# Optimization experiments

Hardware: AMD Instinct MI355X
Metric: run time of the kernel (lower is better)

The kernel has to match this reference:

```python
import jax, jax.numpy as jnp
import numpy as np

HEADS, HEAD_DIM, NQP, NVP = 12, 16, 4, 8
NODE_DIM, EDGE_DIM = 384, 128
B, N = 1, 768


def setup_inputs() -> dict:
    key = jax.random.key(0)
    ks = jax.random.split(key, 12)
    node_features = jax.random.normal(ks[0], (B, N, NODE_DIM), dtype=jnp.float32)
    edge_features = jax.random.normal(ks[1], (B, N, N, EDGE_DIM), dtype=jnp.float32)
    # random valid rotations via QR of gaussian matrices (well-conditioned for inverse)
    A = jax.random.normal(ks[2], (B, N, 3, 3), dtype=jnp.float32)
    Q, _ = jnp.linalg.qr(A)
    R = Q
    t = jax.random.normal(ks[3], (B, N, 3), dtype=jnp.float32)
    def lin(k, din, dout):
        return jax.random.normal(k, (din, dout), dtype=jnp.float32) / np.sqrt(din)
    Wqkv = lin(ks[4], NODE_DIM, 3 * HEADS * HEAD_DIM)
    Wvqk = lin(ks[5], NODE_DIM, 2 * 3 * NQP * HEADS)
    Wvv = lin(ks[6], NODE_DIM, 3 * NVP * HEADS)
    Webias = lin(ks[7], EDGE_DIM, HEADS)
    fin_in = HEADS * EDGE_DIM + HEADS * HEAD_DIM + HEADS * NVP * 4
    Wfin = lin(ks[8], fin_in, NODE_DIM)
    bfin = jnp.zeros((NODE_DIM,), dtype=jnp.float32)
    return {"node_features": node_features, "edge_features": edge_features,
            "R": R, "t": t, "Wqkv": Wqkv, "Wvqk": Wvqk, "Wvv": Wvv,
            "Webias": Webias, "Wfin": Wfin, "bfin": bfin}


def _ipa(node_features, edge_features, R, t, Wqkv, Wvqk, Wvv, Webias, Wfin, bfin):
    b, n, _ = node_features.shape
    h, d, p, pv = HEADS, HEAD_DIM, NQP, NVP
    # scalar q, k, v: [b, h, n, d]
    qkv = (node_features @ Wqkv).reshape(b, n, 3, h, d)
    sq, sk, sv = [jnp.transpose(qkv[:, :, i], (0, 2, 1, 3)) for i in range(3)]
    node_scalar = jnp.einsum('bhid,bhjd->bhij', sq, sk) * (d ** -0.5)
    edge_bias = jnp.einsum('bijd,dh->bhij', edge_features, Webias)
    # vector q/k in local frames: [b, h, n, p, 3]
    vqk = (node_features @ Wvqk).reshape(b, n, 2, h, p, 3)
    vq = jnp.transpose(vqk[:, :, 0], (0, 2, 1, 3, 4))
    vk = jnp.transpose(vqk[:, :, 1], (0, 2, 1, 3, 4))
    t_e = t[:, None, :, None, :]  # [b,1,n,1,3]
    gq = jnp.einsum('bnij,bhnpj->bhnpi', R, vq) + t_e
    gk = jnp.einsum('bnij,bhnpj->bhnpi', R, vk) + t_e
    # ||gk_i - gq_j||^2 summed over (p,3), expanded to avoid [b,h,n,n,p,3]
    wc = np.sqrt(2.0 / 9.0 / p) / 2.0
    k_sq = jnp.sum(gk * gk, axis=(-1, -2))  # [b,h,n]
    q_sq = jnp.sum(gq * gq, axis=(-1, -2))  # [b,h,n]
    cross = jnp.einsum('bhipd,bhjpd->bhij', gk, gq)
    dist = (k_sq[:, :, :, None] + q_sq[:, :, None, :] - 2.0 * cross) * wc
    attn = jax.nn.softmax((node_scalar + edge_bias - dist) * (3 ** -0.5), axis=-1)
    # aggregations
    edge_out = jnp.einsum('bhij,bijd->bihd', attn, edge_features)     # [b,n,h,edge_dim]
    scalar_out = jnp.einsum('bhij,bhjd->bihd', attn, sv)              # [b,n,h,d]
    vv = (node_features @ Wvv).reshape(b, n, h, pv, 3)
    vv = jnp.transpose(vv, (0, 2, 1, 3, 4))                            # [b,h,n,pv,3]
    gvv = jnp.einsum('bnij,bhnpj->bhnpi', R, vv) + t_e
    att_v = jnp.einsum('bhij,bhjpd->bihpd', attn, gvv)                # [b,n,h,pv,3]
    Rinv = jnp.linalg.inv(R)
    local_v = jnp.einsum('bnij,bnhpj->bnhpi', Rinv, att_v - t[:, :, None, None, :])
    v_len = jnp.sqrt(jnp.sum(local_v * local_v, axis=-1))             # [b,n,h,pv]
    combined = jnp.concatenate([
        edge_out.reshape(b, n, -1),
        scalar_out.reshape(b, n, -1),
        local_v.reshape(b, n, -1),
        v_len.reshape(b, n, -1),
    ], axis=-1)
    return node_features + combined @ Wfin + bfin


def reference(node_features, edge_features, R, t, Wqkv, Wvqk, Wvv, Webias, Wfin, bfin):
    return _ipa(node_features, edge_features, R, t, Wqkv, Wvqk, Wvv, Webias, Wfin, bfin)
```

## Files before the change

kernel.cpp:

```cpp
#include <hip/hip_runtime.h>
#include <cmath>


namespace {

constexpr int NN = 768;
constexpr int NH = 12;

constexpr float S3 = 0.5773502691896258f;
constexpr float C1 = 0.25f * S3;
constexpr float C2 = 0.23570226039551584f * S3;
constexpr float C3 = 0.11785113019775792f * S3;

typedef float f32x4 __attribute__((ext_vector_type(4)));
typedef short bf16x8 __attribute__((ext_vector_type(8)));
typedef unsigned int u32x4 __attribute__((ext_vector_type(4)));
typedef unsigned int u32x2 __attribute__((ext_vector_type(2)));
typedef _Float16 f16x2 __attribute__((ext_vector_type(2)));

#define LGKM0 asm volatile("s_waitcnt lgkmcnt(0)" ::: "memory")
#define SCHED0 __builtin_amdgcn_sched_barrier(0)

__device__ inline unsigned cvt_pk_bf16(float lo, float hi) {
  unsigned r;
  asm volatile("v_cvt_pk_bf16_f32 %0, %1, %2" : "=v"(r) : "v"(lo), "v"(hi));
  return r;
}

__device__ inline float fdot2(unsigned a, unsigned b, float c) {
#if __has_builtin(__builtin_amdgcn_fdot2)
  return __builtin_amdgcn_fdot2(__builtin_bit_cast(f16x2, a),
                                __builtin_bit_cast(f16x2, b), c, false);
#else
  union U { unsigned u; _Float16 h[2]; } x, y;
  x.u = a; y.u = b;
  return c + (float)x.h[0] * (float)y.h[0] + (float)x.h[1] * (float)y.h[1];
#endif
}

__device__ inline u32x2 tr_read(unsigned addr) {
  u32x2 d;
  asm volatile("ds_read_b64_tr_b16 %0, %1" : "=v"(d) : "v"(addr));
  return d;
}

__device__ inline f32x4 mfma16(u32x2 a, u32x2 b, f32x4 c) {
  asm volatile("v_mfma_f32_16x16x16_bf16 %0, %1, %2, %0"
               : "+v"(c) : "v"(a), "v"(b));
  return c;
}

__device__ inline unsigned pkf16(float a, float b) {
  union U { _Float16 h[2]; unsigned u; } x;
  x.h[0] = (_Float16)a; x.h[1] = (_Float16)b;
  return x.u;
}

__global__ __launch_bounds__(288) void k_proj(const float* __restrict__ node,
    const float* __restrict__ Wqkv, const float* __restrict__ Wvqk,
    const float* __restrict__ Wvv, float* __restrict__ proj) {
  __shared__ __align__(16) float nl[2][384];
  const int i0 = blockIdx.x * 2;
  const int tid = threadIdx.x;
  for (int idx = tid; idx < 2 * 384; idx += 288)
    ((float*)nl)[idx] = node[(size_t)i0 * 384 + idx];
  __syncthreads();
  const int c0 = tid * 4;
  const float* W; int ld, col;
  if (c0 < 576)      { W = Wqkv; ld = 576; col = c0; }
  else if (c0 < 864) { W = Wvqk; ld = 288; col = c0 - 576; }
  else               { W = Wvv;  ld = 288; col = c0 - 864; }
  float4 acc[2];
#pragma unroll
  for (int r = 0; r < 2; ++r) acc[r] = make_float4(0.f, 0.f, 0.f, 0.f);
#pragma unroll 4
  for (int k = 0; k < 384; ++k) {
    const float4 w4 = *(const float4*)&W[(size_t)k * ld + col];
#pragma unroll
    for (int r = 0; r < 2; ++r) {
      const float nv = nl[r][k];
      acc[r].x += nv * w4.x; acc[r].y += nv * w4.y;
      acc[r].z += nv * w4.z; acc[r].w += nv * w4.w;
    }
  }
#pragma unroll
  for (int r = 0; r < 2; ++r)
    *(float4*)&proj[(size_t)(i0 + r) * 1152 + c0] = acc[r];
}

__global__ __launch_bounds__(256) void k_geom(const float* __restrict__ proj,
    const float* __restrict__ R, const float* __restrict__ t,
    const float* __restrict__ Webias,
    unsigned* __restrict__ Bph, unsigned* __restrict__ Sgh,
    float* __restrict__ V, unsigned* __restrict__ WbP) {
  const int gid = blockIdx.x * 256 + threadIdx.x;
  if (blockIdx.x == 0) {
    const int tid = threadIdx.x;
    const int lane = tid & 63, kk = tid >> 6;
    const int colB = lane & 15, gB = lane >> 4;
    u32x4 wv;
#pragma unroll
    for (int e = 0; e < 4; ++e) {
      const int d = kk * 32 + gB * 8 + 2 * e;
      const float lo = (colB < 12) ? S3 * Webias[d * 12 + colB] : 0.f;
      const float hi = (colB < 12) ? S3 * Webias[(d + 1) * 12 + colB] : 0.f;
      wv[e] = cvt_pk_bf16(lo, hi);
    }
    *(u32x4*)&WbP[(size_t)tid * 4] = wv;
  }
  if (gid >= NN * NH) return;
  const int n = gid / NH, h = gid % NH;
  const float* pr = proj + (size_t)n * 1152;
  const float* Rn = R + n * 9;
  const float t0 = t[n * 3 + 0], t1 = t[n * 3 + 1], t2 = t[n * 3 + 2];
  const size_t hn = (size_t)h * NN + n;
  unsigned* bp = Bph + ((size_t)n * NH + h) * 16;
  unsigned* sg = Sgh + ((size_t)n * NH + h) * 16;
#pragma unroll
  for (int m = 0; m < 8; ++m) {
    bp[m] = pkf16(C1 * pr[(12 + h) * 16 + 2 * m], C1 * pr[(12 + h) * 16 + 2 * m + 1]);
    sg[m] = pkf16(pr[h * 16 + 2 * m], pr[h * 16 + 2 * m + 1]);
    V[hn * 40 + 2 * m]     = pr[(24 + h) * 16 + 2 * m];
    V[hn * 40 + 2 * m + 1] = pr[(24 + h) * 16 + 2 * m + 1];
  }
  float gq[12], gk[12];
  float qs = 0.f, ks = 0.f;
#pragma unroll
  for (int p = 0; p < 4; ++p) {
    {
      const float vx = pr[576 + (h * 4 + p) * 3 + 0];
      const float vy = pr[576 + (h * 4 + p) * 3 + 1];
      const float vz = pr[576 + (h * 4 + p) * 3 + 2];
      const float g0 = Rn[0] * vx + Rn[1] * vy + Rn[2] * vz + t0;
      const float g1 = Rn[3] * vx + Rn[4] * vy + Rn[5] * vz + t1;
      const float g2 = Rn[6] * vx + Rn[7] * vy + Rn[8] * vz + t2;
      gq[p * 3 + 0] = g0; gq[p * 3 + 1] = g1; gq[p * 3 + 2] = g2;
      qs += g0 * g0 + g1 * g1 + g2 * g2;
    }
    {
      const float vx = pr[576 + ((12 + h) * 4 + p) * 3 + 0];
      const float vy = pr[576 + ((12 + h) * 4 + p) * 3 + 1];
      const float vz = pr[576 + ((12 + h) * 4 + p) * 3 + 2];
      const float g0 = Rn[0] * vx + Rn[1] * vy + Rn[2] * vz + t0;
      const float g1 = Rn[3] * vx + Rn[4] * vy + Rn[5] * vz + t1;
      const float g2 = Rn[6] * vx + Rn[7] * vy + Rn[8] * vz + t2;
      gk[p * 3 + 0] = g0; gk[p * 3 + 1] = g1; gk[p * 3 + 2] = g2;
      ks += g0 * g0 + g1 * g1 + g2 * g2;
    }
  }
#pragma unroll
  for (int m = 0; m < 6; ++m) {
    bp[8 + m] = pkf16(C2 * gq[2 * m], C2 * gq[2 * m + 1]);
    sg[8 + m] = pkf16(gk[2 * m], gk[2 * m + 1]);
  }
  bp[14] = pkf16(-C3 * qs, 1.0f);
  sg[14] = pkf16(1.0f, -C3 * ks);
  bp[15] = 0u; sg[15] = 0u;
#pragma unroll
  for (int p = 0; p < 8; ++p) {
    const float vx = pr[864 + (h * 8 + p) * 3 + 0];
    const float vy = pr[864 + (h * 8 + p) * 3 + 1];
    const float vz = pr[864 + (h * 8 + p) * 3 + 2];
    V[hn * 40 + 16 + p * 3 + 0] = Rn[0] * vx + Rn[1] * vy + Rn[2] * vz + t0;
    V[hn * 40 + 16 + p * 3 + 1] = Rn[3] * vx + Rn[4] * vy + Rn[5] * vz + t1;
    V[hn * 40 + 16 + p * 3 + 2] = Rn[6] * vx + Rn[7] * vy + Rn[8] * vz + t2;
  }
}

__global__ __launch_bounds__(256, 4) void k_fused(
    const float* __restrict__ edge, const unsigned* __restrict__ WbP,
    const unsigned* __restrict__ Bph, const unsigned* __restrict__ Sgh,
    unsigned* __restrict__ pTu, float* __restrict__ m_t,
    float* __restrict__ eout, float* __restrict__ msm,
    float* __restrict__ linv) {
  __shared__ __align__(16) unsigned char wreg[4][4224];
  const int i = blockIdx.x;
  const int tid = threadIdx.x;
  const int lane = tid & 63;
  const int w = __builtin_amdgcn_readfirstlane(tid >> 6);
  const int g = lane >> 4;
  const int c16 = lane & 15;
  const int hc = c16 < 12 ? c16 : 11;

  unsigned short* etSw = (unsigned short*)&wreg[w][0];
  const unsigned etbase =
      (unsigned)(uintptr_t)(__attribute__((address_space(3))) unsigned char*)&wreg[w][0];

  float m = -3.0e38f;
  float lsum = 0.f;
  f32x4 acc[8];
#pragma unroll
  for (int dt = 0; dt < 8; ++dt) acc[dt] = (f32x4){0.f, 0.f, 0.f, 0.f};

  float4 ra[8];
  auto load8 = [&](int t) {
    const int jw = t * 64 + w * 16;
#pragma unroll
    for (int q = 0; q < 4; ++q) {
      const int f8 = lane + 64 * q;
      const int j = f8 >> 4, c8 = f8 & 15;
      const float* gp = &edge[((size_t)(i * NN + jw + j)) * 128 + c8 * 8];
      ra[2 * q]     = *(const float4*)gp;
      ra[2 * q + 1] = *(const float4*)(gp + 4);
    }
  };
  auto store8 = [&]() {
#pragma unroll
    for (int q = 0; q < 4; ++q) {
      const int f8 = lane + 64 * q;
      const int j = f8 >> 4, c8 = f8 & 15;
      u32x4 pk;
      pk.x = cvt_pk_bf16(ra[2 * q].x,     ra[2 * q].y);
      pk.y = cvt_pk_bf16(ra[2 * q].z,     ra[2 * q].w);
      pk.z = cvt_pk_bf16(ra[2 * q + 1].x, ra[2 * q + 1].y);
      pk.w = cvt_pk_bf16(ra[2 * q + 1].z, ra[2 * q + 1].w);
      *(u32x4*)&etSw[(c8 >> 1) * 264 + j * 16 + 8 * (c8 & 1)] = pk;
    }
  };

  load8(0);

#pragma unroll 1
  for (int t = 0; t < 12; ++t) {
    const int tw = t * 4 + w;
    LGKM0;
    store8();
    SCHED0;
    if (t < 11) load8(t + 1);

    f32x4 ebacc = {0.f, 0.f, 0.f, 0.f};
#pragma unroll
    for (int kk = 0; kk < 4; ++kk) {
      const int dt = 2 * kk + (g >> 1);
      const bf16x8 a = *(const bf16x8*)&etSw[dt * 264 + c16 * 16 + 8 * (g & 1)];
      const u32x4 wv = *(const u32x4*)&WbP[(size_t)(kk * 64 + lane) * 4];
      const bf16x8 b = __builtin_bit_cast(bf16x8, wv);
      ebacc = __builtin_amdgcn_mfma_f32_16x16x32_bf16(a, b, ebacc, 0, 0, 0);
    }

    const unsigned* sgp = Sgh + ((size_t)i * NH + hc) * 16;
    const u32x4 sg0 = *(const u32x4*)(sgp + 0);
    const u32x4 sg1 = *(const u32x4*)(sgp + 4);
    const u32x4 sg2 = *(const u32x4*)(sgp + 8);
    const u32x4 sg3 = *(const u32x4*)(sgp + 12);
    float lg[4];
#pragma unroll
    for (int r = 0; r < 4; ++r) {
      const unsigned* bpp = Bph + ((size_t)(tw * 16 + 4 * g + r) * NH + hc) * 16;
      const u32x4 b0 = *(const u32x4*)(bpp + 0);
      const u32x4 b1 = *(const u32x4*)(bpp + 4);
      const u32x4 b2 = *(const u32x4*)(bpp + 8);
      const u32x4 b3 = *(const u32x4*)(bpp + 12);
      float a = ebacc[r];
      a = fdot2(b0.x, sg0.x, a); a = fdot2(b0.y, sg0.y, a);
      a = fdot2(b0.z, sg0.z, a); a = fdot2(b0.w, sg0.w, a);
      a = fdot2(b1.x, sg1.x, a); a = fdot2(b1.y, sg1.y, a);
      a = fdot2(b1.z, sg1.z, a); a = fdot2(b1.w, sg1.w, a);
      a = fdot2(b2.x, sg2.x, a); a = fdot2(b2.y, sg2.y, a);
      a = fdot2(b2.z, sg2.z, a); a = fdot2(b2.w, sg2.w, a);
      a = fdot2(b3.x, sg3.x, a); a = fdot2(b3.y, sg3.y, a);
      a = fdot2(b3.z, sg3.z, a);
      lg[r] = a;
    }

    const float lmax = fmaxf(fmaxf(lg[0], lg[1]), fmaxf(lg[2], lg[3]));
    if (__any(lmax > m + 6.f)) {
      float tm = lmax;
      tm = fmaxf(tm, __shfl_xor(tm, 16, 64));
      tm = fmaxf(tm, __shfl_xor(tm, 32, 64));
      const float mn = fmaxf(m, tm);
      const float f = __expf(m - mn);
      m = mn;
      lsum *= f;
      float fr[4];
#pragma unroll
      for (int r = 0; r < 4; ++r) fr[r] = __shfl(f, 4 * g + r, 64);
#pragma unroll
      for (int dt = 0; dt < 8; ++dt) {
        acc[dt][0] *= fr[0]; acc[dt][1] *= fr[1];
        acc[dt][2] *= fr[2]; acc[dt][3] *= fr[3];
      }
    }
    float p0 = __expf(lg[0] - m), p1 = __expf(lg[1] - m);
    float p2 = __expf(lg[2] - m), p3 = __expf(lg[3] - m);
    lsum += (p0 + p1) + (p2 + p3);
    const unsigned pk0 = cvt_pk_bf16(p0, p1);
    const unsigned pk1 = cvt_pk_bf16(p2, p3);
    pTu[((size_t)i * 48 + tw) * 128 + g * 16 + c16]      = pk0;
    pTu[((size_t)i * 48 + tw) * 128 + 64 + g * 16 + c16] = pk1;
    if (g == 0) m_t[((size_t)i * 48 + tw) * 16 + c16] = m;

    u32x2 apk; apk.x = pk0; apk.y = pk1;
    u32x2 bfr[4];
#pragma unroll
    for (int half = 0; half < 2; ++half) {
#pragma unroll
      for (int q = 0; q < 4; ++q)
        bfr[q] = tr_read(etbase + (unsigned)((half * 4 + q) * 528 + g * 128 + c16 * 8));
      LGKM0; SCHED0;
#pragma unroll
      for (int q = 0; q < 4; ++q)
        acc[half * 4 + q] = mfma16(apk, bfr[q], acc[half * 4 + q]);
    }
  }

  {
    unsigned short* OshW = (unsigned short*)&wreg[w][0];
#pragma unroll
    for (int dt = 0; dt < 8; ++dt) {
      u32x2 pkk;
      pkk.x = cvt_pk_bf16(acc[dt][0], acc[dt][1]);
      pkk.y = cvt_pk_bf16(acc[dt][2], acc[dt][3]);
      *(u32x2*)&OshW[dt * 256 + c16 * 16 + g * 4] = pkk;
    }
    float ls = lsum;
    ls += __shfl_xor(ls, 16, 64);
    ls += __shfl_xor(ls, 32, 64);
    if (lane < 16) {
      *(float*)&wreg[w][4096 + lane * 4] = m;
      *(float*)&wreg[w][4160 + lane * 4] = ls;
    }
  }
  __syncthreads();
  for (int idx = tid; idx < 12 * 128; idx += 256) {
    const int h = idx >> 7, d = idx & 127;
    const int dt = d >> 4, dp = d & 15;
    float mv[4], lv[4], Ov[4];
#pragma unroll
    for (int w2 = 0; w2 < 4; ++w2) {
      mv[w2] = *(const float*)&wreg[w2][4096 + h * 4];
      lv[w2] = *(const float*)&wreg[w2][4160 + h * 4];
      const unsigned short us =
          *(const unsigned short*)&wreg[w2][(dt * 256 + dp * 16 + h) * 2];
      Ov[w2] = __uint_as_float(((unsigned)us) << 16);
    }
    const float mb = fmaxf(fmaxf(mv[0], mv[1]), fmaxf(mv[2], mv[3]));
    const float f0 = __expf(mv[0] - mb), f1 = __expf(mv[1] - mb);
    const float f2 = __expf(mv[2] - mb), f3 = __expf(mv[3] - mb);
    const float lb = lv[0] * f0 + lv[1] * f1 + lv[2] * f2 + lv[3] * f3;
    const float O = Ov[0] * f0 + Ov[1] * f1 + Ov[2] * f2 + Ov[3] * f3;
    eout[(size_t)i * 1536 + h * 128 + d] = O / lb;
    if (d == 0) {
      msm[(size_t)h * NN + i] = mb;
      linv[(size_t)h * NN + i] = 1.0f / lb;
    }
  }
}

__global__ __launch_bounds__(320) void k_scav(const unsigned* __restrict__ pTu,
    const float* __restrict__ m_t, const float* __restrict__ msm,
    const float* __restrict__ linv, const float* __restrict__ V,
    float* __restrict__ scav) {
  __shared__ __align__(16) float At[64][20];
  __shared__ __align__(16) float Vt[64][40];
  __shared__ __align__(16) float red[320 * 8];
  const int i0 = blockIdx.x * 16;
  const int h  = blockIdx.y;
  const int tid = threadIdx.x;
  const int js = tid / 80, rem = tid % 80;
  const int rg = rem / 20, cp = rem % 20;
  float2 a0 = {0.f, 0.f}, a1 = {0.f, 0.f}, a2 = {0.f, 0.f}, a3 = {0.f, 0.f};
  for (int jt = 0; jt < 12; ++jt) {
    __syncthreads();
    for (int idx = tid; idx < 1024; idx += 320) {
      const int r = idx >> 6, jj = idx & 63;
      const int i = i0 + r;
      const int tw = jt * 4 + (jj >> 4);
      const int gg = (jj & 15) >> 2, e = jj & 3;
      const unsigned u = pTu[((size_t)i * 48 + tw) * 128 + (e >> 1) * 64 + gg * 16 + h];
      const float p = __uint_as_float((e & 1) ? (u & 0xffff0000u) : (u << 16));
      const float fac = __expf(m_t[((size_t)i * 48 + tw) * 16 + h] - msm[(size_t)h * NN + i])
                      * linv[(size_t)h * NN + i];
      At[jj][r] = p * fac;
    }
    for (int idx = tid; idx < 2560; idx += 320) {
      const int jj = idx / 40, c = idx % 40;
      Vt[jj][c] = V[((size_t)h * NN + jt * 64 + jj) * 40 + c];
    }
    __syncthreads();
#pragma unroll 4
    for (int s = 0; s < 16; ++s) {
      const int jj = js * 16 + s;
      const float4 a4 = *(const float4*)&At[jj][rg * 4];
      const float2 b2 = *(const float2*)&Vt[jj][cp * 2];
      a0.x += a4.x * b2.x; a0.y += a4.x * b2.y;
      a1.x += a4.y * b2.x; a1.y += a4.y * b2.y;
      a2.x += a4.z * b2.x; a2.y += a4.z * b2.y;
      a3.x += a4.w * b2.x; a3.y += a4.w * b2.y;
    }
  }
  __syncthreads();
  *(float4*)&red[tid * 8 + 0] = make_float4(a0.x, a0.y, a1.x, a1.y);
  *(float4*)&red[tid * 8 + 4] = make_float4(a2.x, a2.y, a3.x, a3.y);
  __syncthreads();
  if (tid < 80) {
    const int rg2 = tid / 20, cp2 = tid % 20;
    float4 s0 = make_float4(0.f, 0.f, 0.f, 0.f), s1 = s0;
#pragma unroll
    for (int q = 0; q < 4; ++q) {
      const float4 r0 = *(const float4*)&red[(tid + q * 80) * 8 + 0];
      const float4 r1 = *(const float4*)&red[(tid + q * 80) * 8 + 4];
      s0.x += r0.x; s0.y += r0.y; s0.z += r0.z; s0.w += r0.w;
      s1.x += r1.x; s1.y += r1.y; s1.z += r1.z; s1.w += r1.w;
    }
    const size_t base = (size_t)h * NN + i0 + rg2 * 4;
    *(float2*)&scav[(base + 0) * 40 + cp2 * 2] = make_float2(s0.x, s0.y);
    *(float2*)&scav[(base + 1) * 40 + cp2 * 2] = make_float2(s0.z, s0.w);
    *(float2*)&scav[(base + 2) * 40 + cp2 * 2] = make_float2(s1.x, s1.y);
    *(float2*)&scav[(base + 3) * 40 + cp2 * 2] = make_float2(s1.z, s1.w);
  }
}

__global__ __launch_bounds__(256) void k_comb(
    const float* __restrict__ R, const float* __restrict__ t,
    const float* __restrict__ eout, const float* __restrict__ scav,
    float* __restrict__ comb) {
  const int i0 = blockIdx.x * 4;
  const int tid = threadIdx.x;
  __shared__ float rinv[4][9];
  __shared__ float tl[4][3];
  if (tid < 4) {
    const int i = i0 + tid;
    const float* Rn = R + i * 9;
    const float r00 = Rn[0], r01 = Rn[1], r02 = Rn[2];
    const float r10 = Rn[3], r11 = Rn[4], r12 = Rn[5];
    const float r20 = Rn[6], r21 = Rn[7], r22 = Rn[8];
    const float det = r00 * (r11 * r22 - r12 * r21)
                    - r01 * (r10 * r22 - r12 * r20)
                    + r02 * (r10 * r21 - r11 * r20);
    const float id = 1.0f / det;
    rinv[tid][0] = (r11 * r22 - r12 * r21) * id;
    rinv[tid][1] = (r02 * r21 - r01 * r22) * id;
    rinv[tid][2] = (r01 * r12 - r02 * r11) * id;
    rinv[tid][3] = (r12 * r20 - r10 * r22) * id;
    rinv[tid][4] = (r00 * r22 - r02 * r20) * id;
    rinv[tid][5] = (r02 * r10 - r00 * r12) * id;
    rinv[tid][6] = (r10 * r21 - r11 * r20) * id;
    rinv[tid][7] = (r01 * r20 - r00 * r21) * id;
    rinv[tid][8] = (r00 * r11 - r01 * r10) * id;
    tl[tid][0] = t[i * 3 + 0]; tl[tid][1] = t[i * 3 + 1]; tl[tid][2] = t[i * 3 + 2];
  }
  __syncthreads();
  for (int idx = tid; idx < 4 * 2112; idx += 256) {
    const int r = idx / 2112, k = idx % 2112;
    const int i = i0 + r;
    float val;
    if (k < 1536) {
      val = eout[(size_t)i * 1536 + k];
    } else if (k < 1728) {
      const int s = k - 1536, h = s >> 4, d = s & 15;
      val = scav[((size_t)h * NN + i) * 40 + d];
    } else if (k < 2016) {
      const int s = k - 1728, h = s / 24, rem = s % 24, p = rem / 3, x = rem % 3;
      const float* av = scav + ((size_t)h * NN + i) * 40 + 16 + p * 3;
      const float a0 = av[0] - tl[r][0], a1 = av[1] - tl[r][1], a2 = av[2] - tl[r][2];
      val = rinv[r][x * 3 + 0] * a0 + rinv[r][x * 3 + 1] * a1 + rinv[r][x * 3 + 2] * a2;
    } else {
      const int s = k - 2016, h = s >> 3, p = s & 7;
      const float* av = scav + ((size_t)h * NN + i) * 40 + 16 + p * 3;
      const float a0 = av[0] - tl[r][0], a1 = av[1] - tl[r][1], a2 = av[2] - tl[r][2];
      const float l0 = rinv[r][0] * a0 + rinv[r][1] * a1 + rinv[r][2] * a2;
      const float l1 = rinv[r][3] * a0 + rinv[r][4] * a1 + rinv[r][5] * a2;
      const float l2 = rinv[r][6] * a0 + rinv[r][7] * a1 + rinv[r][8] * a2;
      val = sqrtf(l0 * l0 + l1 * l1 + l2 * l2);
    }
    comb[(size_t)i * 2112 + k] = val;
  }
}

__global__ __launch_bounds__(256) void k_finalA(
    const float* __restrict__ comb, const float* __restrict__ Wfin,
    float* __restrict__ partial) {
  __shared__ __align__(16) float cl[64][36];
  __shared__ __align__(16) float wl[32][68];
  const int i0 = blockIdx.x * 64;
  const int c0 = blockIdx.y * 64;
  const int k0 = blockIdx.z * 192;
  const int tid = threadIdx.x;
  const int cq = tid & 15, rq = tid >> 4;
  float4 acc[4];
#pragma unroll
  for (int r = 0; r < 4; ++r) acc[r] = make_float4(0.f, 0.f, 0.f, 0.f);
  for (int sub = 0; sub < 6; ++sub) {
    const int kc = k0 + sub * 32;
    __syncthreads();
#pragma unroll
    for (int half = 0; half < 2; ++half) {
      const int qi = tid + half * 256;
      const int r = qi >> 3, kq = qi & 7;
      *(float4*)&cl[r][kq * 4] = *(const float4*)&comb[(size_t)(i0 + r) * 2112 + kc + kq * 4];
      const int kk = qi >> 4, cc = qi & 15;
      *(float4*)&wl[kk][cc * 4] = *(const float4*)&Wfin[(size_t)(kc + kk) * 384 + c0 + cc * 4];
    }
    __syncthreads();
#pragma unroll
    for (int k4 = 0; k4 < 8; ++k4) {
      float4 a[4], wv[4];
#pragma unroll
      for (int r = 0; r < 4; ++r) a[r] = *(const float4*)&cl[rq * 4 + r][k4 * 4];
#pragma unroll
      for (int q = 0; q < 4; ++q) wv[q] = *(const float4*)&wl[k4 * 4 + q][cq * 4];
#pragma unroll
      for (int r = 0; r < 4; ++r) {
        acc[r].x += a[r].x * wv[0].x + a[r].y * wv[1].x + a[r].z * wv[2].x + a[r].w * wv[3].x;
        acc[r].y += a[r].x * wv[0].y + a[r].y * wv[1].y + a[r].z * wv[2].y + a[r].w * wv[3].y;
        acc[r].z += a[r].x * wv[0].z + a[r].y * wv[1].z + a[r].z * wv[2].z + a[r].w * wv[3].z;
        acc[r].w += a[r].x * wv[0].w + a[r].y * wv[1].w + a[r].z * wv[2].w + a[r].w * wv[3].w;
      }
    }
  }
#pragma unroll
  for (int r = 0; r < 4; ++r)
    *(float4*)&partial[((size_t)blockIdx.z * NN + i0 + rq * 4 + r) * 384 + c0 + cq * 4] = acc[r];
}

__global__ __launch_bounds__(256) void k_finalB(const float* __restrict__ node,
    const float* __restrict__ partial, const float* __restrict__ bfin,
    float* __restrict__ out) {
  const int gid = blockIdx.x * 256 + threadIdx.x;
  const int i = gid / 96, cq = gid % 96;
  float4 v = *(const float4*)&node[(size_t)i * 384 + cq * 4];
  const float4 b = *(const float4*)&bfin[cq * 4];
  v.x += b.x; v.y += b.y; v.z += b.z; v.w += b.w;
#pragma unroll
  for (int s = 0; s < 11; ++s) {
    const float4 p = *(const float4*)&partial[((size_t)s * NN + i) * 384 + cq * 4];
    v.x += p.x; v.y += p.y; v.z += p.z; v.w += p.w;
  }
  *(float4*)&out[(size_t)i * 384 + cq * 4] = v;
}

}

extern "C" void kernel_launch(void* const* d_in, const int* in_sizes, int n_in,
                              void* d_out, int out_size, void* d_ws, size_t ws_size,
                              hipStream_t stream) {
  const float* node   = (const float*)d_in[0];
  const float* edge   = (const float*)d_in[1];
  const float* R      = (const float*)d_in[2];
  const float* t      = (const float*)d_in[3];
  const float* Wqkv   = (const float*)d_in[4];
  const float* Wvqk   = (const float*)d_in[5];
  const float* Wvv    = (const float*)d_in[6];
  const float* Webias = (const float*)d_in[7];
  const float* Wfin   = (const float*)d_in[8];
  const float* bfin   = (const float*)d_in[9];
  float* out = (float*)d_out;

  float* ws = (float*)d_ws;
  float*    proj = ws;
  float*    V    = proj + 884736;
  unsigned* Bph  = (unsigned*)(V + 368640);
  unsigned* Sgh  = Bph + 147456;
  unsigned* WbP  = Sgh + 147456;
  unsigned* pTu  = WbP + 1024;
  float*    m_t  = (float*)(pTu + 4718592);
  float*    eout = m_t + 589824;
  float*    scav = eout + 1179648;
  float*    msm  = scav + 368640;
  float*    linv = msm + 9216;
  float* comb    = (float*)pTu;
  float* partial = comb + 1622016;

  hipLaunchKernelGGL(k_proj, dim3(384), dim3(288), 0, stream,
                     node, Wqkv, Wvqk, Wvv, proj);
  hipLaunchKernelGGL(k_geom, dim3(36), dim3(256), 0, stream,
                     proj, R, t, Webias, Bph, Sgh, V, WbP);
  hipLaunchKernelGGL(k_fused, dim3(768), dim3(256), 0, stream,
                     edge, WbP, Bph, Sgh, pTu, m_t, eout, msm, linv);
  hipLaunchKernelGGL(k_scav, dim3(48, 12), dim3(320), 0, stream,
                     pTu, m_t, msm, linv, V, scav);
  hipLaunchKernelGGL(k_comb, dim3(192), dim3(256), 0, stream,
                     R, t, eout, scav, comb);
  hipLaunchKernelGGL(k_finalA, dim3(12, 6, 11), dim3(256), 0, stream,
                     comb, Wfin, partial);
  hipLaunchKernelGGL(k_finalB, dim3(288), dim3(256), 0, stream,
                     node, partial, bfin, out);
}
```

Baseline: 256.1 us.

## Read eout directly in final GEMM, hoist loop-invariant loads, retile projection

k_comb no longer copies the 1536-column eout block into the combined buffer. k_finalA now reads eout directly for its first eight K-slices and a smaller 576-wide combX buffer for the rest, which removes one full write and re-read of eout. In k_fused, the Webias MFMA fragments and the Sgh vectors are loaded once before the tile loop rather than on every iteration, and the launch-bounds occupancy hint drops from 4 to 3 to make room for the extra registers. k_proj handles 8 rows per block instead of 2 to get more reuse of each weight load, which leaves only 96 blocks and so less parallelism.

```diff
diff --git a/kernel.cpp b/kernel.cpp
--- a/kernel.cpp
+++ b/kernel.cpp
@@ -59,10 +59,10 @@
 __global__ __launch_bounds__(288) void k_proj(const float* __restrict__ node,
     const float* __restrict__ Wqkv, const float* __restrict__ Wvqk,
     const float* __restrict__ Wvv, float* __restrict__ proj) {
-  __shared__ __align__(16) float nl[2][384];
-  const int i0 = blockIdx.x * 2;
+  __shared__ __align__(16) float nl[8][384];
+  const int i0 = blockIdx.x * 8;
   const int tid = threadIdx.x;
-  for (int idx = tid; idx < 2 * 384; idx += 288)
+  for (int idx = tid; idx < 8 * 384; idx += 288)
     ((float*)nl)[idx] = node[(size_t)i0 * 384 + idx];
   __syncthreads();
   const int c0 = tid * 4;
@@ -70,21 +70,21 @@
   if (c0 < 576)      { W = Wqkv; ld = 576; col = c0; }
   else if (c0 < 864) { W = Wvqk; ld = 288; col = c0 - 576; }
   else               { W = Wvv;  ld = 288; col = c0 - 864; }
-  float4 acc[2];
-#pragma unroll
-  for (int r = 0; r < 2; ++r) acc[r] = make_float4(0.f, 0.f, 0.f, 0.f);
+  float4 acc[8];
+#pragma unroll
+  for (int r = 0; r < 8; ++r) acc[r] = make_float4(0.f, 0.f, 0.f, 0.f);
 #pragma unroll 4
   for (int k = 0; k < 384; ++k) {
     const float4 w4 = *(const float4*)&W[(size_t)k * ld + col];
 #pragma unroll
-    for (int r = 0; r < 2; ++r) {
+    for (int r = 0; r < 8; ++r) {
       const float nv = nl[r][k];
       acc[r].x += nv * w4.x; acc[r].y += nv * w4.y;
       acc[r].z += nv * w4.z; acc[r].w += nv * w4.w;
     }
   }
 #pragma unroll
-  for (int r = 0; r < 2; ++r)
+  for (int r = 0; r < 8; ++r)
     *(float4*)&proj[(size_t)(i0 + r) * 1152 + c0] = acc[r];
 }
 
@@ -167,7 +167,7 @@
   }
 }
 
-__global__ __launch_bounds__(256, 4) void k_fused(
+__global__ __launch_bounds__(256, 3) void k_fused(
     const float* __restrict__ edge, const unsigned* __restrict__ WbP,
     const unsigned* __restrict__ Bph, const unsigned* __restrict__ Sgh,
     unsigned* __restrict__ pTu, float* __restrict__ m_t,
@@ -186,6 +186,18 @@
   const unsigned etbase =
       (unsigned)(uintptr_t)(__attribute__((address_space(3))) unsigned char*)&wreg[w][0];
 
+  bf16x8 wbfrag[4];
+#pragma unroll
+  for (int kk = 0; kk < 4; ++kk)
+    wbfrag[kk] = __builtin_bit_cast(bf16x8,
+        *(const u32x4*)&WbP[(size_t)(kk * 64 + lane) * 4]);
+
+  const unsigned* sgp = Sgh + ((size_t)i * NH + hc) * 16;
+  const u32x4 sg0 = *(const u32x4*)(sgp + 0);
+  const u32x4 sg1 = *(const u32x4*)(sgp + 4);
+  const u32x4 sg2 = *(const u32x4*)(sgp + 8);
+  const u32x4 sg3 = *(const u32x4*)(sgp + 12);
+
   float m = -3.0e38f;
   float lsum = 0.f;
   f32x4 acc[8];
@@ -233,16 +245,9 @@
     for (int kk = 0; kk < 4; ++kk) {
       const int dt = 2 * kk + (g >> 1);
       const bf16x8 a = *(const bf16x8*)&etSw[dt * 264 + c16 * 16 + 8 * (g & 1)];
-      const u32x4 wv = *(const u32x4*)&WbP[(size_t)(kk * 64 + lane) * 4];
-      const bf16x8 b = __builtin_bit_cast(bf16x8, wv);
-      ebacc = __builtin_amdgcn_mfma_f32_16x16x32_bf16(a, b, ebacc, 0, 0, 0);
-    }
-
-    const unsigned* sgp = Sgh + ((size_t)i * NH + hc) * 16;
-    const u32x4 sg0 = *(const u32x4*)(sgp + 0);
-    const u32x4 sg1 = *(const u32x4*)(sgp + 4);
-    const u32x4 sg2 = *(const u32x4*)(sgp + 8);
-    const u32x4 sg3 = *(const u32x4*)(sgp + 12);
+      ebacc = __builtin_amdgcn_mfma_f32_16x16x32_bf16(a, wbfrag[kk], ebacc, 0, 0, 0);
+    }
+
     float lg[4];
 #pragma unroll
     for (int r = 0; r < 4; ++r) {
@@ -251,8 +256,8 @@
       const u32x4 b1 = *(const u32x4*)(bpp + 4);
       const u32x4 b2 = *(const u32x4*)(bpp + 8);
       const u32x4 b3 = *(const u32x4*)(bpp + 12);
-      float a = ebacc[r];
-      a = fdot2(b0.x, sg0.x, a); a = fdot2(b0.y, sg0.y, a);
+      float a = fdot2(b0.x, sg0.x, 0.f);
+      a = fdot2(b0.y, sg0.y, a);
       a = fdot2(b0.z, sg0.z, a); a = fdot2(b0.w, sg0.w, a);
       a = fdot2(b1.x, sg1.x, a); a = fdot2(b1.y, sg1.y, a);
       a = fdot2(b1.z, sg1.z, a); a = fdot2(b1.w, sg1.w, a);
@@ -260,7 +265,7 @@
       a = fdot2(b2.z, sg2.z, a); a = fdot2(b2.w, sg2.w, a);
       a = fdot2(b3.x, sg3.x, a); a = fdot2(b3.y, sg3.y, a);
       a = fdot2(b3.z, sg3.z, a);
-      lg[r] = a;
+      lg[r] = a + ebacc[r];
     }
 
     const float lmax = fmaxf(fmaxf(lg[0], lg[1]), fmaxf(lg[2], lg[3]));
@@ -413,8 +418,7 @@
 
 __global__ __launch_bounds__(256) void k_comb(
     const float* __restrict__ R, const float* __restrict__ t,
-    const float* __restrict__ eout, const float* __restrict__ scav,
-    float* __restrict__ comb) {
+    const float* __restrict__ scav, float* __restrict__ combX) {
   const int i0 = blockIdx.x * 4;
   const int tid = threadIdx.x;
   __shared__ float rinv[4][9];
@@ -441,22 +445,20 @@
     tl[tid][0] = t[i * 3 + 0]; tl[tid][1] = t[i * 3 + 1]; tl[tid][2] = t[i * 3 + 2];
   }
   __syncthreads();
-  for (int idx = tid; idx < 4 * 2112; idx += 256) {
-    const int r = idx / 2112, k = idx % 2112;
+  for (int idx = tid; idx < 4 * 576; idx += 256) {
+    const int r = idx / 576, k2 = idx % 576;
     const int i = i0 + r;
     float val;
-    if (k < 1536) {
-      val = eout[(size_t)i * 1536 + k];
-    } else if (k < 1728) {
-      const int s = k - 1536, h = s >> 4, d = s & 15;
+    if (k2 < 192) {
+      const int h = k2 >> 4, d = k2 & 15;
       val = scav[((size_t)h * NN + i) * 40 + d];
-    } else if (k < 2016) {
-      const int s = k - 1728, h = s / 24, rem = s % 24, p = rem / 3, x = rem % 3;
+    } else if (k2 < 480) {
+      const int s = k2 - 192, h = s / 24, rem = s % 24, p = rem / 3, x = rem % 3;
       const float* av = scav + ((size_t)h * NN + i) * 40 + 16 + p * 3;
       const float a0 = av[0] - tl[r][0], a1 = av[1] - tl[r][1], a2 = av[2] - tl[r][2];
       val = rinv[r][x * 3 + 0] * a0 + rinv[r][x * 3 + 1] * a1 + rinv[r][x * 3 + 2] * a2;
     } else {
-      const int s = k - 2016, h = s >> 3, p = s & 7;
+      const int s = k2 - 480, h = s >> 3, p = s & 7;
       const float* av = scav + ((size_t)h * NN + i) * 40 + 16 + p * 3;
       const float a0 = av[0] - tl[r][0], a1 = av[1] - tl[r][1], a2 = av[2] - tl[r][2];
       const float l0 = rinv[r][0] * a0 + rinv[r][1] * a1 + rinv[r][2] * a2;
@@ -464,33 +466,38 @@
       const float l2 = rinv[r][6] * a0 + rinv[r][7] * a1 + rinv[r][8] * a2;
       val = sqrtf(l0 * l0 + l1 * l1 + l2 * l2);
     }
-    comb[(size_t)i * 2112 + k] = val;
+    combX[(size_t)i * 576 + k2] = val;
   }
 }
 
 __global__ __launch_bounds__(256) void k_finalA(
-    const float* __restrict__ comb, const float* __restrict__ Wfin,
-    float* __restrict__ partial) {
+    const float* __restrict__ eout, const float* __restrict__ combX,
+    const float* __restrict__ Wfin, float* __restrict__ partial) {
   __shared__ __align__(16) float cl[64][36];
   __shared__ __align__(16) float wl[32][68];
   const int i0 = blockIdx.x * 64;
   const int c0 = blockIdx.y * 64;
   const int k0 = blockIdx.z * 192;
+  const float* src; int stride, koff;
+  if (blockIdx.z < 8) { src = eout;  stride = 1536; koff = k0; }
+  else                { src = combX; stride = 576;  koff = k0 - 1536; }
   const int tid = threadIdx.x;
   const int cq = tid & 15, rq = tid >> 4;
   float4 acc[4];
 #pragma unroll
   for (int r = 0; r < 4; ++r) acc[r] = make_float4(0.f, 0.f, 0.f, 0.f);
   for (int sub = 0; sub < 6; ++sub) {
-    const int kc = k0 + sub * 32;
+    const int kc = sub * 32;
     __syncthreads();
 #pragma unroll
     for (int half = 0; half < 2; ++half) {
       const int qi = tid + half * 256;
       const int r = qi >> 3, kq = qi & 7;
-      *(float4*)&cl[r][kq * 4] = *(const float4*)&comb[(size_t)(i0 + r) * 2112 + kc + kq * 4];
+      *(float4*)&cl[r][kq * 4] =
+          *(const float4*)&src[(size_t)(i0 + r) * stride + koff + kc + kq * 4];
       const int kk = qi >> 4, cc = qi & 15;
-      *(float4*)&wl[kk][cc * 4] = *(const float4*)&Wfin[(size_t)(kc + kk) * 384 + c0 + cc * 4];
+      *(float4*)&wl[kk][cc * 4] =
+          *(const float4*)&Wfin[(size_t)(k0 + kc + kk) * 384 + c0 + cc * 4];
     }
     __syncthreads();
 #pragma unroll
@@ -559,10 +566,10 @@
   float*    scav = eout + 1179648;
   float*    msm  = scav + 368640;
   float*    linv = msm + 9216;
-  float* comb    = (float*)pTu;
-  float* partial = comb + 1622016;
-
-  hipLaunchKernelGGL(k_proj, dim3(384), dim3(288), 0, stream,
+  float* combX   = (float*)pTu;
+  float* partial = combX + 442368;
+
+  hipLaunchKernelGGL(k_proj, dim3(96), dim3(288), 0, stream,
                      node, Wqkv, Wvqk, Wvv, proj);
   hipLaunchKernelGGL(k_geom, dim3(36), dim3(256), 0, stream,
                      proj, R, t, Webias, Bph, Sgh, V, WbP);
@@ -571,9 +578,9 @@
   hipLaunchKernelGGL(k_scav, dim3(48, 12), dim3(320), 0, stream,
                      pTu, m_t, msm, linv, V, scav);
   hipLaunchKernelGGL(k_comb, dim3(192), dim3(256), 0, stream,
-                     R, t, eout, scav, comb);
+                     R, t, scav, combX);
   hipLaunchKernelGGL(k_finalA, dim3(12, 6, 11), dim3(256), 0, stream,
-                     comb, Wfin, partial);
+                     eout, combX, Wfin, partial);
   hipLaunchKernelGGL(k_finalB, dim3(288), dim3(256), 0, stream,
                      node, partial, bfin, out);
 }
```

After: 358.1 us. 1.4x slower.
